# Performance work log

Measured on AMD Instinct MI355X. Metric: run time of the kernel, lower is better.

Reference implementation:

```python
import jax, jax.numpy as jnp
import numpy as np

VOL = (64, 64, 64)
EPS = 1e-06
B, T, C, H, W = 2, 128, 1, 256, 256


def setup_inputs() -> dict:
    key = jax.random.key(0)
    k1, k2, k3, k4 = jax.random.split(key, 4)
    slices = jax.random.normal(k1, (B, T, C, H, W), dtype=jnp.float32)
    # translation coords at half-integer grid positions inside the volume so
    # min distance to any voxel is ~0.866 (keeps exp(1/d) finite in fp32)
    trans_xyz = jax.random.randint(k2, (B, T, 3), 0, VOL[0]).astype(jnp.float32) + 0.5
    rot = jax.random.normal(k3, (B, T, 3), dtype=jnp.float32)
    transforms = jnp.concatenate([trans_xyz, rot], axis=-1)  # [B, T, 6]
    slice_indices = jax.random.randint(k4, (B, T), 0, T)
    return {"slices": slices, "transforms": transforms, "slice_indices": slice_indices}


def reference(slices, transforms, slice_indices):
    vx, vy, vz = VOL
    V = vx * vy * vz
    b, t, c, h, w = slices.shape
    # gather selected transforms [B,T,D] and slices [B,T,C,H,W]
    sel_t = jnp.take_along_axis(transforms, slice_indices[:, :, None], axis=1)
    sel_s = jnp.take_along_axis(
        slices, slice_indices[:, :, None, None, None], axis=1)
    # voxel grid coords [V,3] (meshgrid 'ij')
    gx, gy, gz = jnp.meshgrid(jnp.arange(vx), jnp.arange(vy), jnp.arange(vz), indexing="ij")
    grid = jnp.stack([gx, gy, gz], axis=-1).reshape(V, 3).astype(slices.dtype)
    slice_coords = sel_t[..., :3]  # [B,T,3]
    # distances [B,T,V]
    diff = grid[None, None, :, :] - slice_coords[:, :, None, :]
    dist = jnp.sqrt(jnp.sum(diff * diff, axis=-1))
    wgt = jnp.exp(1.0 / (dist + EPS))
    wgt = wgt / jnp.sum(wgt, axis=1, keepdims=True)  # normalize over slices T
    # (W^T @ I).mean over HW == W^T @ mean(I) by linearity
    intensity_mean = sel_s.reshape(b, t, -1).mean(axis=-1)  # [B,T]
    recon = jnp.einsum("btv,bt->bv", wgt, intensity_mean)  # [B,V]
    return recon.reshape(b, 1, vx, vy, vz)
```

## Files before the change

kernel.cpp:

```cpp
#include <hip/hip_runtime.h>

#define VCNT 262144
#define NB 2
#define NT 128
#define HWPIX 65536
#define LN2  0.69314718055994531f
#define LN2X2 1.38629436111989062f

typedef float f32x2 __attribute__((ext_vector_type(2)));

static __device__ __forceinline__ float fast_exp2(float x) {
#if __has_builtin(__builtin_amdgcn_exp2f)
    return __builtin_amdgcn_exp2f(x);
#else
    float r; asm("v_exp_f32 %0, %1" : "=v"(r) : "v"(x)); return r;
#endif
}
static __device__ __forceinline__ float fast_rsq(float x) {
#if __has_builtin(__builtin_amdgcn_rsqf)
    return __builtin_amdgcn_rsqf(x);
#else
    float r; asm("v_rsq_f32 %0, %1" : "=v"(r) : "v"(x)); return r;
#endif
}

__global__ __launch_bounds__(256) void slice_partial_kernel(
    const float* __restrict__ slices, const int* __restrict__ sidx,
    float* __restrict__ partials)
{
    const int s   = blockIdx.x >> 3;
    const int b   = s >> 7;
    const int tsl = s & 127;

    __shared__ int needed;
    if (threadIdx.x == 0) needed = 0;
    __syncthreads();
    if (threadIdx.x < NT && sidx[(b << 7) + threadIdx.x] == tsl) needed = 1;
    __syncthreads();
    if (!needed) return;

    const int j = blockIdx.x & 7;
    const float4* p = (const float4*)(slices + (size_t)s * HWPIX) + j * 2048;

    float acc = 0.0f;
#pragma unroll
    for (int i = 0; i < 8; ++i) {
        float4 v = p[i * 256 + threadIdx.x];
        acc += (v.x + v.y) + (v.z + v.w);
    }
#pragma unroll
    for (int off = 32; off > 0; off >>= 1)
        acc += __shfl_down(acc, off, 64);

    __shared__ float ws[4];
    const int lane = threadIdx.x & 63;
    const int wid  = threadIdx.x >> 6;
    if (lane == 0) ws[wid] = acc;
    __syncthreads();
    if (threadIdx.x == 0)
        partials[blockIdx.x] = (ws[0] + ws[1]) + (ws[2] + ws[3]);
}

__global__ __launch_bounds__(256) void recon_kernel(
    const float* __restrict__ transforms,
    const int*   __restrict__ sidx,
    const float* __restrict__ partials,
    float*       __restrict__ out)
{
    __shared__ float4 ct[NT];
    __shared__ float  kk[NT];
    __shared__ int    cnt[NT];
    __shared__ int    wcnt[2];
    __shared__ int    ncnt;

    const int tid = threadIdx.x;
    const int b   = blockIdx.x >> 8;
    const int v0  = ((blockIdx.x & 255) << 10) + (tid << 2);

    if (tid < NT) cnt[tid] = 0;
    __syncthreads();
    if (tid < NT) atomicAdd(&cnt[sidx[(b << 7) + tid]], 1);
    __syncthreads();

    const int  k      = (tid < NT) ? cnt[tid] : 0;
    const bool neededf = (k > 0);
    const unsigned long long mask = __ballot(neededf);
    const int lane = tid & 63;
    const int wid  = tid >> 6;
    if (tid < NT && lane == 0) wcnt[wid] = (int)__popcll(mask);
    __syncthreads();
    if (neededf) {
        const int pos = (int)__popcll(mask & ((1ull << lane) - 1ull))
                      + (wid ? wcnt[0] : 0);
        const float* tr = transforms + (size_t)((b << 7) + tid) * 6;
        const float* pp = partials   + (size_t)((b << 7) + tid) * 8;
        float m = 0.0f;
#pragma unroll
        for (int i = 0; i < 8; ++i) m += pp[i];
        m *= (1.0f / (float)HWPIX);
        const float fk = (float)k;
        ct[pos] = make_float4(tr[0] * LN2, tr[1] * LN2, tr[2] * LN2, fk * m);
        kk[pos] = fk;
    }
    if (tid == 0) ncnt = wcnt[0] + wcnt[1];
    __syncthreads();
    const int n = ncnt;

    const float fx  = (float)(v0 >> 12) * LN2;
    const float fy  = (float)((v0 >> 6) & 63) * LN2;
    const float fz0 = (float)(v0 & 63) * LN2;
    const f32x2 fzp = {fz0, fz0 + LN2};

    f32x2 wsumA = {0.0f, 0.0f}, accA = {0.0f, 0.0f};
    f32x2 wsumB = {0.0f, 0.0f}, accB = {0.0f, 0.0f};

#pragma unroll 2
    for (int t = 0; t < n; ++t) {
        const float4 c  = ct[t];
        const float  kf = kk[t];
        const float dx = fx - c.x;
        const float dy = fy - c.y;
        const float base = fmaf(dy, dy, dx * dx);
        f32x2 dz0 = fzp - c.z;
        f32x2 d2a = dz0 * dz0 + base;
        f32x2 dz1 = dz0 + LN2X2;
        f32x2 d2b = dz1 * dz1 + base;

        f32x2 wA, wB;
        wA.x = fast_exp2(fast_rsq(d2a.x));
        wA.y = fast_exp2(fast_rsq(d2a.y));
        wB.x = fast_exp2(fast_rsq(d2b.x));
        wB.y = fast_exp2(fast_rsq(d2b.y));

        wsumA += wA * kf;
        accA  += wA * c.w;
        wsumB += wB * kf;
        accB  += wB * c.w;
    }

    float4 o;
    o.x = accA.x / wsumA.x;
    o.y = accA.y / wsumA.y;
    o.z = accB.x / wsumB.x;
    o.w = accB.y / wsumB.y;
    *(float4*)(out + (size_t)b * VCNT + v0) = o;
}

extern "C" void kernel_launch(void* const* d_in, const int* in_sizes, int n_in,
                              void* d_out, int out_size, void* d_ws, size_t ws_size,
                              hipStream_t stream)
{
    const float* slices     = (const float*)d_in[0];
    const float* transforms = (const float*)d_in[1];
    const int*   sidx       = (const int*)d_in[2];
    float* out      = (float*)d_out;
    float* partials = (float*)d_ws;

    slice_partial_kernel<<<NB * NT * 8, 256, 0, stream>>>(slices, sidx, partials);
    recon_kernel<<<NB * VCNT / 1024, 256, 0, stream>>>(transforms, sidx, partials, out);
}
```

Measured before the change: 26.64 us.

## Replace per-voxel exp(rsqrt) with shared-memory lookup table and linear interpolation

Builds a 641-entry table of exp(1/sqrt(d2)) in LDS per block, indexed by the float exponent and top mantissa bits of the squared distance, and linearly interpolates it instead of issuing two transcendental instructions per voxel-slice pair. For small distances (d2<16) it falls back to the exact rsq/exp2 path, under a wave-uniform branch. The table is filled with double-precision exp/sqrt per block. This trades transcendental-unit work for LDS gathers, extra integer ops and possible bank conflicts, and it adds approximation error from the interpolation.

```diff
diff --git a/kernel.cpp b/kernel.cpp
--- a/kernel.cpp
+++ b/kernel.cpp
@@ -4,8 +4,7 @@
 #define NB 2
 #define NT 128
 #define HWPIX 65536
-#define LN2  0.69314718055994531f
-#define LN2X2 1.38629436111989062f
+#define LOG2E 1.44269504088896340f
 
 typedef float f32x2 __attribute__((ext_vector_type(2)));
 
@@ -61,6 +60,8 @@
         partials[blockIdx.x] = (ws[0] + ws[1]) + (ws[2] + ws[3]);
 }
 
+#define TBL_N 641
+
 __global__ __launch_bounds__(256) void recon_kernel(
     const float* __restrict__ transforms,
     const int*   __restrict__ sidx,
@@ -72,21 +73,29 @@
     __shared__ int    cnt[NT];
     __shared__ int    wcnt[2];
     __shared__ int    ncnt;
+    __shared__ float  tbl[TBL_N];
 
-    const int tid = threadIdx.x;
-    const int b   = blockIdx.x >> 8;
-    const int v0  = ((blockIdx.x & 255) << 10) + (tid << 2);
+    const int tid  = threadIdx.x;
+    const int lane = tid & 63;
+    const int wid  = tid >> 6;
+    const int b    = blockIdx.x >> 8;
+    const int v0   = ((blockIdx.x & 255) << 10) + (tid << 2);
 
     if (tid < NT) cnt[tid] = 0;
     __syncthreads();
+
     if (tid < NT) atomicAdd(&cnt[sidx[(b << 7) + tid]], 1);
+#pragma unroll
+    for (int i = tid; i < TBL_N; i += 256) {
+        const int e = i >> 6, f = i & 63;
+        const float d2v = __uint_as_float((unsigned)((131 + e) << 23) | (unsigned)(f << 17));
+        tbl[i] = (float)exp(1.0 / sqrt((double)d2v));
+    }
     __syncthreads();
 
-    const int  k      = (tid < NT) ? cnt[tid] : 0;
+    const int  k       = (tid < NT) ? cnt[tid] : 0;
     const bool neededf = (k > 0);
     const unsigned long long mask = __ballot(neededf);
-    const int lane = tid & 63;
-    const int wid  = tid >> 6;
     if (tid < NT && lane == 0) wcnt[wid] = (int)__popcll(mask);
     __syncthreads();
     if (neededf) {
@@ -99,17 +108,17 @@
         for (int i = 0; i < 8; ++i) m += pp[i];
         m *= (1.0f / (float)HWPIX);
         const float fk = (float)k;
-        ct[pos] = make_float4(tr[0] * LN2, tr[1] * LN2, tr[2] * LN2, fk * m);
+        ct[pos] = make_float4(tr[0], tr[1], tr[2], fk * m);
         kk[pos] = fk;
     }
     if (tid == 0) ncnt = wcnt[0] + wcnt[1];
     __syncthreads();
     const int n = ncnt;
 
-    const float fx  = (float)(v0 >> 12) * LN2;
-    const float fy  = (float)((v0 >> 6) & 63) * LN2;
-    const float fz0 = (float)(v0 & 63) * LN2;
-    const f32x2 fzp = {fz0, fz0 + LN2};
+    const float fx = (float)(v0 >> 12);
+    const float fy = (float)((v0 >> 6) & 63);
+    const float fz = (float)(v0 & 63);
+    const f32x2 fzp = {fz, fz + 1.0f};
 
     f32x2 wsumA = {0.0f, 0.0f}, accA = {0.0f, 0.0f};
     f32x2 wsumB = {0.0f, 0.0f}, accB = {0.0f, 0.0f};
@@ -122,20 +131,47 @@
         const float dy = fy - c.y;
         const float base = fmaf(dy, dy, dx * dx);
         f32x2 dz0 = fzp - c.z;
-        f32x2 d2a = dz0 * dz0 + base;
-        f32x2 dz1 = dz0 + LN2X2;
-        f32x2 d2b = dz1 * dz1 + base;
+        f32x2 dz1 = dz0 + 2.0f;
+        f32x2 d2a, d2b;
+        d2a.x = fmaf(dz0.x, dz0.x, base);  d2a.y = fmaf(dz0.y, dz0.y, base);
+        d2b.x = fmaf(dz1.x, dz1.x, base);  d2b.y = fmaf(dz1.y, dz1.y, base);
 
-        f32x2 wA, wB;
-        wA.x = fast_exp2(fast_rsq(d2a.x));
-        wA.y = fast_exp2(fast_rsq(d2a.y));
-        wB.x = fast_exp2(fast_rsq(d2b.x));
-        wB.y = fast_exp2(fast_rsq(d2b.y));
+        float w0, w1, w2, w3;
+        {
+            const unsigned b0 = __float_as_uint(d2a.x);
+            const unsigned b1 = __float_as_uint(d2a.y);
+            const unsigned b2 = __float_as_uint(d2b.x);
+            const unsigned b3 = __float_as_uint(d2b.y);
+            int i0 = (int)(b0 >> 17) - 8384; i0 = i0 < 0 ? 0 : i0;
+            int i1 = (int)(b1 >> 17) - 8384; i1 = i1 < 0 ? 0 : i1;
+            int i2 = (int)(b2 >> 17) - 8384; i2 = i2 < 0 ? 0 : i2;
+            int i3 = (int)(b3 >> 17) - 8384; i3 = i3 < 0 ? 0 : i3;
+            const float f0 = (float)(b0 & 0x1FFFF) * (1.0f / 131072.0f);
+            const float f1 = (float)(b1 & 0x1FFFF) * (1.0f / 131072.0f);
+            const float f2 = (float)(b2 & 0x1FFFF) * (1.0f / 131072.0f);
+            const float f3 = (float)(b3 & 0x1FFFF) * (1.0f / 131072.0f);
+            const float a0 = tbl[i0], c0 = tbl[i0 + 1];
+            const float a1 = tbl[i1], c1 = tbl[i1 + 1];
+            const float a2 = tbl[i2], c2 = tbl[i2 + 1];
+            const float a3 = tbl[i3], c3 = tbl[i3 + 1];
+            w0 = fmaf(f0, c0 - a0, a0);
+            w1 = fmaf(f1, c1 - a1, a1);
+            w2 = fmaf(f2, c2 - a2, a2);
+            w3 = fmaf(f3, c3 - a3, a3);
+        }
 
-        wsumA += wA * kf;
-        accA  += wA * c.w;
-        wsumB += wB * kf;
-        accB  += wB * c.w;
+        const float mn = fminf(fminf(d2a.x, d2a.y), fminf(d2b.x, d2b.y));
+        if (__any(mn < 16.0f)) {
+            w0 = (d2a.x < 16.0f) ? fast_exp2(fast_rsq(d2a.x) * LOG2E) : w0;
+            w1 = (d2a.y < 16.0f) ? fast_exp2(fast_rsq(d2a.y) * LOG2E) : w1;
+            w2 = (d2b.x < 16.0f) ? fast_exp2(fast_rsq(d2b.x) * LOG2E) : w2;
+            w3 = (d2b.y < 16.0f) ? fast_exp2(fast_rsq(d2b.y) * LOG2E) : w3;
+        }
+
+        wsumA.x = fmaf(w0, kf, wsumA.x);  wsumA.y = fmaf(w1, kf, wsumA.y);
+        wsumB.x = fmaf(w2, kf, wsumB.x);  wsumB.y = fmaf(w3, kf, wsumB.y);
+        accA.x  = fmaf(w0, c.w, accA.x);  accA.y  = fmaf(w1, c.w, accA.y);
+        accB.x  = fmaf(w2, c.w, accB.x);  accB.y  = fmaf(w3, c.w, accB.y);
     }
 
     float4 o;
```

After: 38.14 us. 43.2% more time.

## Split slice loop across 4 lane groups, 8 voxels per thread, shuffle-reduce

Applied to the files above, without the earlier changes.

The recon kernel now gives each thread 8 voxels instead of 4 and splits the loop over needed slices across 4 lane groups of 16 within a wave. Partial weight sums are combined with xor shuffles, and one lane group writes the outputs. The grid doubles to 1024 blocks, so the per-block setup (histogram, compaction, mean) is repeated more often. The goal is more parallelism and more independent transcendental chains per iteration, at the cost of extra shuffles, idle lanes during the store, and duplicated block setup.

```diff
diff --git a/kernel.cpp b/kernel.cpp
--- a/kernel.cpp
+++ b/kernel.cpp
@@ -4,8 +4,10 @@
 #define NB 2
 #define NT 128
 #define HWPIX 65536
-#define LN2  0.69314718055994531f
+#define LN2   0.69314718055994531f
 #define LN2X2 1.38629436111989062f
+#define LN2X4 2.77258872223978124f
+#define LN2X6 4.15888308335967186f
 
 typedef float f32x2 __attribute__((ext_vector_type(2)));
 
@@ -73,20 +75,19 @@
     __shared__ int    wcnt[2];
     __shared__ int    ncnt;
 
-    const int tid = threadIdx.x;
-    const int b   = blockIdx.x >> 8;
-    const int v0  = ((blockIdx.x & 255) << 10) + (tid << 2);
+    const int tid  = threadIdx.x;
+    const int lane = tid & 63;
+    const int wid  = tid >> 6;
+    const int b    = blockIdx.x >> 9;
 
     if (tid < NT) cnt[tid] = 0;
     __syncthreads();
     if (tid < NT) atomicAdd(&cnt[sidx[(b << 7) + tid]], 1);
     __syncthreads();
 
-    const int  k      = (tid < NT) ? cnt[tid] : 0;
+    const int  k       = (tid < NT) ? cnt[tid] : 0;
     const bool neededf = (k > 0);
     const unsigned long long mask = __ballot(neededf);
-    const int lane = tid & 63;
-    const int wid  = tid >> 6;
     if (tid < NT && lane == 0) wcnt[wid] = (int)__popcll(mask);
     __syncthreads();
     if (neededf) {
@@ -106,44 +107,63 @@
     __syncthreads();
     const int n = ncnt;
 
+    const int g   = (lane >> 4) & 3;
+    const int col = (wid << 4) + (lane & 15);
+    const int v0  = ((blockIdx.x & 511) << 9) + (col << 3);
+
     const float fx  = (float)(v0 >> 12) * LN2;
     const float fy  = (float)((v0 >> 6) & 63) * LN2;
     const float fz0 = (float)(v0 & 63) * LN2;
     const f32x2 fzp = {fz0, fz0 + LN2};
 
-    f32x2 wsumA = {0.0f, 0.0f}, accA = {0.0f, 0.0f};
-    f32x2 wsumB = {0.0f, 0.0f}, accB = {0.0f, 0.0f};
+    f32x2 ws0 = {0,0}, ws1 = {0,0}, ws2 = {0,0}, ws3 = {0,0};
+    f32x2 ac0 = {0,0}, ac1 = {0,0}, ac2 = {0,0}, ac3 = {0,0};
 
 #pragma unroll 2
-    for (int t = 0; t < n; ++t) {
+    for (int t = g; t < n; t += 4) {
         const float4 c  = ct[t];
         const float  kf = kk[t];
         const float dx = fx - c.x;
         const float dy = fy - c.y;
         const float base = fmaf(dy, dy, dx * dx);
-        f32x2 dz0 = fzp - c.z;
-        f32x2 d2a = dz0 * dz0 + base;
-        f32x2 dz1 = dz0 + LN2X2;
-        f32x2 d2b = dz1 * dz1 + base;
 
-        f32x2 wA, wB;
-        wA.x = fast_exp2(fast_rsq(d2a.x));
-        wA.y = fast_exp2(fast_rsq(d2a.y));
-        wB.x = fast_exp2(fast_rsq(d2b.x));
-        wB.y = fast_exp2(fast_rsq(d2b.y));
+        f32x2 d0 = fzp - c.z;
+        f32x2 d1 = d0 + LN2X2;
+        f32x2 d2 = d0 + LN2X4;
+        f32x2 d3 = d0 + LN2X6;
+        f32x2 q0 = d0 * d0 + base;
+        f32x2 q1 = d1 * d1 + base;
+        f32x2 q2 = d2 * d2 + base;
+        f32x2 q3 = d3 * d3 + base;
 
-        wsumA += wA * kf;
-        accA  += wA * c.w;
-        wsumB += wB * kf;
-        accB  += wB * c.w;
+        f32x2 w0, w1, w2, w3;
+        w0.x = fast_exp2(fast_rsq(q0.x));  w0.y = fast_exp2(fast_rsq(q0.y));
+        w1.x = fast_exp2(fast_rsq(q1.x));  w1.y = fast_exp2(fast_rsq(q1.y));
+        w2.x = fast_exp2(fast_rsq(q2.x));  w2.y = fast_exp2(fast_rsq(q2.y));
+        w3.x = fast_exp2(fast_rsq(q3.x));  w3.y = fast_exp2(fast_rsq(q3.y));
+
+        ws0 += w0 * kf;   ac0 += w0 * c.w;
+        ws1 += w1 * kf;   ac1 += w1 * c.w;
+        ws2 += w2 * kf;   ac2 += w2 * c.w;
+        ws3 += w3 * kf;   ac3 += w3 * c.w;
     }
 
-    float4 o;
-    o.x = accA.x / wsumA.x;
-    o.y = accA.y / wsumA.y;
-    o.z = accB.x / wsumB.x;
-    o.w = accB.y / wsumB.y;
-    *(float4*)(out + (size_t)b * VCNT + v0) = o;
+#define CMB(r) r.x += __shfl_xor(r.x, 16, 64); r.y += __shfl_xor(r.y, 16, 64); \
+               r.x += __shfl_xor(r.x, 32, 64); r.y += __shfl_xor(r.y, 32, 64);
+    CMB(ws0) CMB(ws1) CMB(ws2) CMB(ws3)
+    CMB(ac0) CMB(ac1) CMB(ac2) CMB(ac3)
+#undef CMB
+
+    if ((lane & 48) == 0) {
+        float4 oa, ob;
+        oa.x = ac0.x / ws0.x;  oa.y = ac0.y / ws0.y;
+        oa.z = ac1.x / ws1.x;  oa.w = ac1.y / ws1.y;
+        ob.x = ac2.x / ws2.x;  ob.y = ac2.y / ws2.y;
+        ob.z = ac3.x / ws3.x;  ob.w = ac3.y / ws3.y;
+        float* o = out + (size_t)b * VCNT + v0;
+        *(float4*)o       = oa;
+        *(float4*)(o + 4) = ob;
+    }
 }
 
 extern "C" void kernel_launch(void* const* d_in, const int* in_sizes, int n_in,
@@ -157,5 +177,5 @@
     float* partials = (float*)d_ws;
 
     slice_partial_kernel<<<NB * NT * 8, 256, 0, stream>>>(slices, sidx, partials);
-    recon_kernel<<<NB * VCNT / 1024, 256, 0, stream>>>(transforms, sidx, partials, out);
+    recon_kernel<<<NB * VCNT / 512, 256, 0, stream>>>(transforms, sidx, partials, out);
 }
```

After: 25.54 us. 1.04x faster.
